# Kernel tuning notes

Measured on AMD Instinct MI355X. Metric: run time of the kernel, lower is better.

## Reference

```python
import jax, jax.numpy as jnp
import numpy as np

D_MODEL = 512
N_HEADS = 8
MAX_CH = 128
LN_EPS = 1e-5


def setup_inputs() -> dict:
    key = jax.random.key(0)
    ks = jax.random.split(key, 8)
    B, T, C, D = 8, 256, 64, D_MODEL
    x = jax.random.normal(ks[0], (B, T, C, D), dtype=jnp.float32)
    # nn.MultiheadAttention params: packed in_proj [3D, D], out_proj [D, D]
    in_proj_w = jax.random.normal(ks[1], (3 * D, D), dtype=jnp.float32) * 0.02
    in_proj_b = jnp.zeros((3 * D,), dtype=jnp.float32)
    out_proj_w = jax.random.normal(ks[2], (D, D), dtype=jnp.float32) * 0.02
    out_proj_b = jnp.zeros((D,), dtype=jnp.float32)
    ln_g = jnp.ones((D,), dtype=jnp.float32)
    ln_b = jnp.zeros((D,), dtype=jnp.float32)
    rel_pos_bias = jax.random.normal(ks[3], (N_HEADS, MAX_CH, MAX_CH), dtype=jnp.float32) * 0.02
    return {"x": x, "in_proj_w": in_proj_w, "in_proj_b": in_proj_b,
            "out_proj_w": out_proj_w, "out_proj_b": out_proj_b,
            "ln_g": ln_g, "ln_b": ln_b, "rel_pos_bias": rel_pos_bias}


def _layernorm(x, g, b):
    mu = jnp.mean(x, axis=-1, keepdims=True)
    var = jnp.var(x, axis=-1, keepdims=True)
    return (x - mu) * jax.lax.rsqrt(var + LN_EPS) * g + b


def reference(x, in_proj_w, in_proj_b, out_proj_w, out_proj_b, ln_g, ln_b, rel_pos_bias):
    B, T, C, D = x.shape
    H = N_HEADS
    hd = D // H
    N = B * T
    xf = x.reshape(N, C, D)
    # 2D additive attn_mask: mean over heads of rel-pos bias, broadcast over heads/batch
    bias = jnp.mean(rel_pos_bias[:, :C, :C], axis=0)  # [C, C]
    qkv = xf @ in_proj_w.T + in_proj_b  # [N, C, 3D]
    q, k, v = jnp.split(qkv, 3, axis=-1)
    q = q.reshape(N, C, H, hd)
    k = k.reshape(N, C, H, hd)
    v = v.reshape(N, C, H, hd)
    scores = jnp.einsum('nqhd,nkhd->nhqk', q, k) / jnp.sqrt(jnp.float32(hd))
    scores = scores + bias[None, None, :, :]
    attn = jax.nn.softmax(scores, axis=-1)
    ctx = jnp.einsum('nhqk,nkhd->nqhd', attn, v).reshape(N, C, D)
    attn_out = ctx @ out_proj_w.T + out_proj_b
    out = _layernorm(xf + attn_out, ln_g, ln_b)
    return out.reshape(B, T, C, D)
```

## Files before the change

kernel.cpp:

```cpp
#include <hip/hip_runtime.h>
#include <stdint.h>
#include <stddef.h>


typedef __attribute__((ext_vector_type(8))) short short8;
typedef __attribute__((ext_vector_type(4))) float f32x4;

typedef __attribute__((address_space(3))) unsigned int as3_u32;
typedef __attribute__((address_space(1))) unsigned int as1_u32;

#define VMCNT8 asm volatile("s_waitcnt vmcnt(8)" ::: "memory")
#define VMCNT5 asm volatile("s_waitcnt vmcnt(5)" ::: "memory")
#define VMCNT4 asm volatile("s_waitcnt vmcnt(4)" ::: "memory")
#define VMCNT0 asm volatile("s_waitcnt vmcnt(0)" ::: "memory")
#define LGKM0  asm volatile("s_waitcnt lgkmcnt(0)" ::: "memory")
#define BARR() __builtin_amdgcn_s_barrier()
#define PRIO1  __builtin_amdgcn_s_setprio(1)
#define PRIO0  __builtin_amdgcn_s_setprio(0)

__device__ __forceinline__ unsigned short f2bf(float f) {
  unsigned u = __builtin_bit_cast(unsigned, f);
  u = (u + 0x7FFFu + ((u >> 16) & 1u)) >> 16;
  return (unsigned short)u;
}

__device__ __forceinline__ f32x4 mfma16(short8 a, short8 b, f32x4 c) {
  return __builtin_amdgcn_mfma_f32_16x16x32_bf16(a, b, c, 0, 0, 0);
}

__device__ __forceinline__ short8 rd8s(const char* buf, int row, int unit) {
  return *(const short8*)(buf + row * 128 + ((unit ^ (row & 7)) * 16));
}
__device__ __forceinline__ void wr2s(char* buf, int row, int col, unsigned short v) {
  int slot = (col >> 3) ^ (row & 7);
  *(unsigned short*)(buf + row * 128 + slot * 16 + (col & 7) * 2) = v;
}
__device__ __forceinline__ void wr8s(char* buf, int row, int col, uint2 v) {
  int slot = (col >> 3) ^ (row & 7);
  *(uint2*)(buf + row * 128 + slot * 16 + (col & 7) * 2) = v;
}

__device__ __forceinline__ void stage16k(char* ldsbase, const char* gsrc, int w, int lane) {
#pragma unroll
  for (int j = 0; j < 4; ++j) {
    int off = j * 4096 + w * 1024;
    __builtin_amdgcn_global_load_lds((const as1_u32*)(gsrc + off + lane * 16),
                                     (as3_u32*)(ldsbase + off), 16, 0, 0);
  }
}

__global__ void prep_kernel(const float* __restrict__ wqkv_f,
                            const float* __restrict__ wo_f,
                            const float* __restrict__ rel,
                            unsigned short* __restrict__ wt,
                            float* __restrict__ bias2d) {
  int b = blockIdx.x, tid = threadIdx.x;
  if (b < 128) {
    unsigned short* dst = wt + (size_t)b * 8192;
#pragma unroll
    for (int t = 0; t < 4; ++t) {
      int u = t * 256 + tid;
      int row = u >> 4, us = u & 15;
      int kg = (us & 8) | ((us ^ row) & 7);
      const float* src;
      if (b < 96) {
        int h = b / 12, i = b % 12;
        int rg = i >> 2, kc = i & 3;
        src = wqkv_f + (size_t)(rg * 512 + h * 64 + row) * 512 + kc * 128 + kg * 8;
      } else {
        int cw = b - 96;
        int kc = cw >> 3, ng = cw & 7;
        src = wo_f + (size_t)(ng * 64 + row) * 512 + kc * 128 + kg * 8;
      }
      float4 a = *(const float4*)src;
      float4 c = *(const float4*)(src + 4);
      unsigned p0 = (unsigned)f2bf(a.x) | ((unsigned)f2bf(a.y) << 16);
      unsigned p1 = (unsigned)f2bf(a.z) | ((unsigned)f2bf(a.w) << 16);
      unsigned p2 = (unsigned)f2bf(c.x) | ((unsigned)f2bf(c.y) << 16);
      unsigned p3 = (unsigned)f2bf(c.z) | ((unsigned)f2bf(c.w) << 16);
      *(uint4*)(dst + u * 8) = make_uint4(p0, p1, p2, p3);
    }
  } else {
    int idx = (b - 128) * 256 + tid;
    int m = idx >> 6, nn = idx & 63;
    float s = 0.f;
#pragma unroll
    for (int hh = 0; hh < 8; ++hh) s += rel[hh * 16384 + m * 128 + nn];
    bias2d[idx] = s * 0.125f;
  }
}

__global__ __launch_bounds__(256)
__attribute__((amdgpu_waves_per_eu(2, 2))) void attn_qkv(
    const float* __restrict__ x,
    const char* __restrict__ wq,
    const float* __restrict__ bqkv,
    const float* __restrict__ bias2d,
    char* __restrict__ ctxg) {
  extern __shared__ __attribute__((aligned(16))) char smem[];
  char* WS = smem;
  char* B0 = smem + 49152;
  char* B1 = smem + 57344;
  char* B2 = smem + 65536;
  float* BQ = (float*)(smem + 73728);

  const int n = blockIdx.x;
  const int tid = threadIdx.x;
  const int w = tid >> 6, lane = tid & 63;
  const int l15 = lane & 15, g = lane >> 4;
  const int wm = w >> 1, wn = w & 1;
  const int mrow = w * 16 + g * 4;
  const int wrow = w * 16 + l15;

#pragma unroll
  for (int i = 0; i < 6; ++i) BQ[i * 256 + tid] = bqkv[i * 256 + tid];

  short8 xf[32];
#pragma unroll
  for (int mt = 0; mt < 2; ++mt) {
    const float* xr = x + ((size_t)n * 64 + wm * 32 + mt * 16 + l15) * 512;
#pragma unroll
    for (int kk = 0; kk < 16; ++kk) {
      float4 a = *(const float4*)(xr + kk * 32 + g * 8);
      float4 c = *(const float4*)(xr + kk * 32 + g * 8 + 4);
      short8 s;
      s[0] = (short)f2bf(a.x); s[1] = (short)f2bf(a.y);
      s[2] = (short)f2bf(a.z); s[3] = (short)f2bf(a.w);
      s[4] = (short)f2bf(c.x); s[5] = (short)f2bf(c.y);
      s[6] = (short)f2bf(c.z); s[7] = (short)f2bf(c.w);
      xf[mt * 16 + kk] = s;
    }
  }
  float b2d[16];
#pragma unroll
  for (int nt = 0; nt < 4; ++nt)
#pragma unroll
    for (int r = 0; r < 4; ++r)
      b2d[nt * 4 + r] = bias2d[(mrow + r) * 64 + nt * 16 + l15];

  LGKM0; BARR();

  stage16k(WS, wq, w, lane);
  stage16k(WS + 16384, wq + 16384, w, lane);

  int b = 0, cur = 0;
  for (int h = 0; h < 8; ++h) {
    float bq2[2], bk2[2], bv2[2];
#pragma unroll
    for (int nt = 0; nt < 2; ++nt) {
      int col = h * 64 + wn * 32 + nt * 16 + l15;
      bq2[nt] = BQ[col];
      bk2[nt] = BQ[512 + col];
      bv2[nt] = BQ[1024 + col];
    }
#pragma unroll
    for (int rg = 0; rg < 3; ++rg) {
      f32x4 acc[2][2] = {};
#pragma unroll
      for (int c = 0; c < 4; ++c) {
        int tgt = cur + 2; if (tgt >= 3) tgt -= 3;
        if (b + 2 < 96) {
          stage16k(WS + tgt * 16384, wq + (size_t)(b + 2) * 16384, w, lane);
          VMCNT8;
        } else if (b + 1 < 96) { VMCNT4; } else { VMCNT0; }
        BARR();
        const char* ws = WS + cur * 16384;
        PRIO1;
#pragma unroll
        for (int ks = 0; ks < 4; ++ks) {
#pragma unroll
          for (int nt = 0; nt < 2; ++nt) {
            int row = wn * 32 + nt * 16 + l15;
            int kg = ks * 4 + g;
            int us = (kg & 8) | ((kg ^ row) & 7);
            short8 bfr = *(const short8*)(ws + row * 256 + us * 16);
            acc[0][nt] = mfma16(xf[c * 4 + ks], bfr, acc[0][nt]);
            acc[1][nt] = mfma16(xf[16 + c * 4 + ks], bfr, acc[1][nt]);
          }
        }
        PRIO0;
        BARR();
        ++b; ++cur; if (cur >= 3) cur -= 3;
      }
      if (rg == 0) {
#pragma unroll
        for (int mt = 0; mt < 2; ++mt)
#pragma unroll
          for (int nt = 0; nt < 2; ++nt)
#pragma unroll
            for (int r = 0; r < 4; ++r)
              wr2s(B0, wm * 32 + mt * 16 + g * 4 + r, wn * 32 + nt * 16 + l15,
                   f2bf(acc[mt][nt][r] + bq2[nt]));
      } else if (rg == 1) {
#pragma unroll
        for (int mt = 0; mt < 2; ++mt)
#pragma unroll
          for (int nt = 0; nt < 2; ++nt)
#pragma unroll
            for (int r = 0; r < 4; ++r)
              wr2s(B1, wm * 32 + mt * 16 + g * 4 + r, wn * 32 + nt * 16 + l15,
                   f2bf(acc[mt][nt][r] + bk2[nt]));
      } else {
#pragma unroll
        for (int mt = 0; mt < 2; ++mt)
#pragma unroll
          for (int nt = 0; nt < 2; ++nt) {
            unsigned short p0 = f2bf(acc[mt][nt][0] + bv2[nt]);
            unsigned short p1 = f2bf(acc[mt][nt][1] + bv2[nt]);
            unsigned short p2 = f2bf(acc[mt][nt][2] + bv2[nt]);
            unsigned short p3 = f2bf(acc[mt][nt][3] + bv2[nt]);
            unsigned lo = (unsigned)p0 | ((unsigned)p1 << 16);
            unsigned hi = (unsigned)p2 | ((unsigned)p3 << 16);
            wr8s(B2, wn * 32 + nt * 16 + l15, wm * 32 + mt * 16 + g * 4,
                 make_uint2(lo, hi));
          }
      }
    }
    LGKM0; BARR();

    {
      f32x4 sc[4] = {};
      short8 aq0 = rd8s(B0, wrow, g);
      short8 aq1 = rd8s(B0, wrow, 4 + g);
#pragma unroll
      for (int nt = 0; nt < 4; ++nt)
        sc[nt] = mfma16(aq0, rd8s(B1, nt * 16 + l15, g), sc[nt]);
#pragma unroll
      for (int nt = 0; nt < 4; ++nt)
        sc[nt] = mfma16(aq1, rd8s(B1, nt * 16 + l15, 4 + g), sc[nt]);
      float mx[4] = {-1e30f, -1e30f, -1e30f, -1e30f};
#pragma unroll
      for (int nt = 0; nt < 4; ++nt)
#pragma unroll
        for (int r = 0; r < 4; ++r) {
          float v = sc[nt][r] * 0.125f + b2d[nt * 4 + r];
          sc[nt][r] = v;
          mx[r] = fmaxf(mx[r], v);
        }
#pragma unroll
      for (int mk = 1; mk < 16; mk <<= 1)
#pragma unroll
        for (int r = 0; r < 4; ++r) mx[r] = fmaxf(mx[r], __shfl_xor(mx[r], mk));
      float sm[4] = {0.f, 0.f, 0.f, 0.f};
#pragma unroll
      for (int nt = 0; nt < 4; ++nt)
#pragma unroll
        for (int r = 0; r < 4; ++r) {
          float e = __expf(sc[nt][r] - mx[r]);
          sc[nt][r] = e;
          sm[r] += e;
        }
#pragma unroll
      for (int mk = 1; mk < 16; mk <<= 1)
#pragma unroll
        for (int r = 0; r < 4; ++r) sm[r] += __shfl_xor(sm[r], mk);
      float inv[4];
#pragma unroll
      for (int r = 0; r < 4; ++r) inv[r] = 1.0f / sm[r];
#pragma unroll
      for (int nt = 0; nt < 4; ++nt)
#pragma unroll
        for (int r = 0; r < 4; ++r)
          wr2s(B0, mrow + r, nt * 16 + l15, f2bf(sc[nt][r] * inv[r]));
    }

    f32x4 cv[4] = {};
    {
      short8 ap0 = rd8s(B0, wrow, g);
      short8 ap1 = rd8s(B0, wrow, 4 + g);
#pragma unroll
      for (int nt = 0; nt < 4; ++nt)
        cv[nt] = mfma16(ap0, rd8s(B2, nt * 16 + l15, g), cv[nt]);
#pragma unroll
      for (int nt = 0; nt < 4; ++nt)
        cv[nt] = mfma16(ap1, rd8s(B2, nt * 16 + l15, 4 + g), cv[nt]);
    }
    BARR();
#pragma unroll
    for (int nt = 0; nt < 4; ++nt)
#pragma unroll
      for (int r = 0; r < 4; ++r)
        wr2s(B1, mrow + r, nt * 16 + l15, f2bf(cv[nt][r]));
    LGKM0; BARR();

    {
      char* cdst = ctxg + (size_t)n * 131072 + h * 8192;
#pragma unroll
      for (int it = 0; it < 2; ++it) {
        int flat = it * 256 + tid;
        int row = flat >> 3, s = flat & 7;
        uint4 v = *(const uint4*)(B1 + row * 128 + s * 16);
        *(uint4*)(cdst + row * 128 + s * 16) = v;
      }
    }
  }
}

__global__ __launch_bounds__(256)
__attribute__((amdgpu_waves_per_eu(2, 2))) void oproj_ln(
    const char* __restrict__ ctxg,
    const char* __restrict__ wo,
    const float* __restrict__ bo,
    const float* __restrict__ x,
    const float* __restrict__ lng,
    const float* __restrict__ lnb,
    float* __restrict__ out) {
  __shared__ __attribute__((aligned(16))) char smem[65536];
  char* WB = smem;
  char* CB = smem + 32768;
  float* EP  = (float*)smem;
  float* SM1 = (float*)(smem + 32768);
  float* SM2 = (float*)(smem + 33408);

  const int n = blockIdx.x;
  const int tid = threadIdx.x;
  const int w = tid >> 6, lane = tid & 63;
  const int l15 = lane & 15, g = lane >> 4;
  const int um = w >> 1, un = w & 1;

  const char* cbase = ctxg + (size_t)n * 131072;

  stage16k(CB, cbase, w, lane);
  stage16k(WB, wo, w, lane);

  f32x4 acc[8][2][2] = {};

  for (int kc = 0; kc < 4; ++kc) {
    short8 actx[2][4];
#pragma unroll
    for (int ng = 0; ng < 8; ++ng) {
      int b = kc * 8 + ng;
      if (b < 31)
        stage16k(WB + (((b + 1) & 1) << 14), wo + (size_t)(b + 1) * 16384, w, lane);
      if ((ng & 1) == 0 && kc < 3) {
        int p = ng >> 1;
        int off = p * 4096 + w * 1024;
        __builtin_amdgcn_global_load_lds(
            (const as1_u32*)(cbase + (kc + 1) * 16384 + off + lane * 16),
            (as3_u32*)(CB + (((kc + 1) & 1) << 14) + off), 16, 0, 0);
      }
      if (b < 31) { VMCNT5; } else { VMCNT0; }
      BARR();
      const char* cb = CB + ((kc & 1) << 14);
      if (ng == 0) {
#pragma unroll
        for (int mt = 0; mt < 2; ++mt)
#pragma unroll
          for (int ks = 0; ks < 4; ++ks) {
            int row = um * 32 + mt * 16 + l15;
            int u = ks * 4 + g;
            actx[mt][ks] = *(const short8*)(cb + (u >> 3) * 8192 + row * 128 +
                                            (((u & 7) ^ (row & 7)) * 16));
          }
      }
      const char* ws = WB + ((b & 1) << 14);
      PRIO1;
#pragma unroll
      for (int ks = 0; ks < 4; ++ks) {
#pragma unroll
        for (int nt = 0; nt < 2; ++nt) {
          int row = un * 32 + nt * 16 + l15;
          int kg = ks * 4 + g;
          int us = (kg & 8) | ((kg ^ row) & 7);
          short8 bfr = *(const short8*)(ws + row * 256 + us * 16);
          acc[ng][0][nt] = mfma16(actx[0][ks], bfr, acc[ng][0][nt]);
          acc[ng][1][nt] = mfma16(actx[1][ks], bfr, acc[ng][1][nt]);
        }
      }
      PRIO0;
      BARR();
    }
  }

  VMCNT0;
  const float* xblk = x + (size_t)n * 32768;
  float* oblk = out + (size_t)n * 32768;
  float s1[2][4] = {}, s2[2][4] = {};

#pragma unroll
  for (int ng = 0; ng < 8; ++ng) {
#pragma unroll
    for (int t = 0; t < 4; ++t) {
      int flat = t * 256 + tid;
      int row = flat >> 4, f4 = flat & 15;
      float4 v = *(const float4*)(xblk + row * 512 + ng * 64 + f4 * 4);
      *(float4*)(EP + row * 68 + f4 * 4) = v;
    }
    LGKM0; BARR();
    float boA[2];
#pragma unroll
    for (int nt = 0; nt < 2; ++nt) boA[nt] = bo[ng * 64 + un * 32 + nt * 16 + l15];
#pragma unroll
    for (int mt = 0; mt < 2; ++mt)
#pragma unroll
      for (int nt = 0; nt < 2; ++nt)
#pragma unroll
        for (int r = 0; r < 4; ++r) {
          int row = um * 32 + mt * 16 + g * 4 + r;
          float xv = EP[row * 68 + un * 32 + nt * 16 + l15];
          float v = acc[ng][mt][nt][r] + boA[nt] + xv;
          acc[ng][mt][nt][r] = v;
          s1[mt][r] += v;
          s2[mt][r] += v * v;
        }
    LGKM0; BARR();
  }
#pragma unroll
  for (int mk = 1; mk < 16; mk <<= 1)
#pragma unroll
    for (int mt = 0; mt < 2; ++mt)
#pragma unroll
      for (int r = 0; r < 4; ++r) {
        s1[mt][r] += __shfl_xor(s1[mt][r], mk);
        s2[mt][r] += __shfl_xor(s2[mt][r], mk);
      }
  if (l15 == 0) {
#pragma unroll
    for (int mt = 0; mt < 2; ++mt)
#pragma unroll
      for (int r = 0; r < 4; ++r) {
        int row = um * 32 + mt * 16 + g * 4 + r;
        SM1[row * 2 + un] = s1[mt][r];
        SM2[row * 2 + un] = s2[mt][r];
      }
  }
  LGKM0; BARR();
  float mu[2][4], rs[2][4];
#pragma unroll
  for (int mt = 0; mt < 2; ++mt)
#pragma unroll
    for (int r = 0; r < 4; ++r) {
      int row = um * 32 + mt * 16 + g * 4 + r;
      float a1 = SM1[row * 2] + SM1[row * 2 + 1];
      float a2 = SM2[row * 2] + SM2[row * 2 + 1];
      float m = a1 * (1.0f / 512.0f);
      float var = a2 * (1.0f / 512.0f) - m * m;
      mu[mt][r] = m;
      rs[mt][r] = rsqrtf(var + 1e-5f);
    }
  BARR();
#pragma unroll
  for (int ng = 0; ng < 8; ++ng) {
    float lgA[2], lbA[2];
#pragma unroll
    for (int nt = 0; nt < 2; ++nt) {
      int col = ng * 64 + un * 32 + nt * 16 + l15;
      lgA[nt] = lng[col];
      lbA[nt] = lnb[col];
    }
#pragma unroll
    for (int mt = 0; mt < 2; ++mt)
#pragma unroll
      for (int nt = 0; nt < 2; ++nt)
#pragma unroll
        for (int r = 0; r < 4; ++r) {
          int row = um * 32 + mt * 16 + g * 4 + r;
          EP[row * 68 + un * 32 + nt * 16 + l15] =
              (acc[ng][mt][nt][r] - mu[mt][r]) * rs[mt][r] * lgA[nt] + lbA[nt];
        }
    LGKM0; BARR();
#pragma unroll
    for (int t = 0; t < 4; ++t) {
      int flat = t * 256 + tid;
      int row = flat >> 4, f4 = flat & 15;
      *(float4*)(oblk + row * 512 + ng * 64 + f4 * 4) =
          *(const float4*)(EP + row * 68 + f4 * 4);
    }
    BARR();
  }
}

extern "C" void kernel_launch(void* const* d_in, const int* in_sizes, int n_in,
                              void* d_out, int out_size, void* d_ws, size_t ws_size,
                              hipStream_t stream) {
  const float* x    = (const float*)d_in[0];
  const float* wqkv = (const float*)d_in[1];
  const float* bqkv = (const float*)d_in[2];
  const float* wo   = (const float*)d_in[3];
  const float* bo   = (const float*)d_in[4];
  const float* lng  = (const float*)d_in[5];
  const float* lnb  = (const float*)d_in[6];
  const float* rel  = (const float*)d_in[7];

  unsigned short* wt = (unsigned short*)d_ws;
  float* bias2d = (float*)((char*)d_ws + 128 * 16384);
  const char* wqc = (const char*)d_ws;
  const char* woc = (const char*)d_ws + 96 * 16384;

  hipFuncSetAttribute(reinterpret_cast<const void*>(attn_qkv),
                      hipFuncAttributeMaxDynamicSharedMemorySize, 79872);

  prep_kernel<<<144, 256, 0, stream>>>(wqkv, wo, rel, wt, bias2d);
  attn_qkv<<<2048, 256, 79872, stream>>>(x, wqc, bqkv, bias2d, (char*)d_out);
  oproj_ln<<<2048, 256, 0, stream>>>((const char*)d_out, woc, bo, x, lng, lnb,
                                     (float*)d_out);
}
```

Baseline: 559.4 us.

## Pre-convert x to bf16 in prep kernel and stream it through LDS

Moves the fp32-to-bf16 conversion of x into the prep kernel, which writes a swizzled bf16 copy into the scratch half of the output buffer. The attention kernel then streams x k-chunks through LDS instead of holding 32 short8 x fragments in registers. It reorders the QKV GEMM so q, k and v accumulate together per k-chunk with double-buffered weight staging. This frees registers and drops the per-block conversion, at the cost of an extra global write and read of x in bf16, more barriers and full vmcnt(0) waits that weaken the prefetch overlap.

```diff
diff --git a/kernel.cpp b/kernel.cpp
--- a/kernel.cpp
+++ b/kernel.cpp
@@ -9,9 +9,7 @@
 typedef __attribute__((address_space(3))) unsigned int as3_u32;
 typedef __attribute__((address_space(1))) unsigned int as1_u32;
 
-#define VMCNT8 asm volatile("s_waitcnt vmcnt(8)" ::: "memory")
 #define VMCNT5 asm volatile("s_waitcnt vmcnt(5)" ::: "memory")
-#define VMCNT4 asm volatile("s_waitcnt vmcnt(4)" ::: "memory")
 #define VMCNT0 asm volatile("s_waitcnt vmcnt(0)" ::: "memory")
 #define LGKM0  asm volatile("s_waitcnt lgkmcnt(0)" ::: "memory")
 #define BARR() __builtin_amdgcn_s_barrier()
@@ -49,29 +47,25 @@
   }
 }
 
-__global__ void prep_kernel(const float* __restrict__ wqkv_f,
+__global__ void prep_kernel(const float* __restrict__ x,
+                            const float* __restrict__ wqkv_f,
                             const float* __restrict__ wo_f,
                             const float* __restrict__ rel,
                             unsigned short* __restrict__ wt,
-                            float* __restrict__ bias2d) {
+                            float* __restrict__ bias2d,
+                            char* __restrict__ dout) {
   int b = blockIdx.x, tid = threadIdx.x;
-  if (b < 128) {
-    unsigned short* dst = wt + (size_t)b * 8192;
+  if (b < 8192) {
+    int n = b >> 2, kc = b & 3;
+    unsigned short* dst =
+        (unsigned short*)(dout + (size_t)n * 131072 + 65536 + kc * 16384);
+    const float* src0 = x + (size_t)n * 32768 + kc * 128;
 #pragma unroll
     for (int t = 0; t < 4; ++t) {
       int u = t * 256 + tid;
       int row = u >> 4, us = u & 15;
       int kg = (us & 8) | ((us ^ row) & 7);
-      const float* src;
-      if (b < 96) {
-        int h = b / 12, i = b % 12;
-        int rg = i >> 2, kc = i & 3;
-        src = wqkv_f + (size_t)(rg * 512 + h * 64 + row) * 512 + kc * 128 + kg * 8;
-      } else {
-        int cw = b - 96;
-        int kc = cw >> 3, ng = cw & 7;
-        src = wo_f + (size_t)(ng * 64 + row) * 512 + kc * 128 + kg * 8;
-      }
+      const float* src = src0 + row * 512 + kg * 8;
       float4 a = *(const float4*)src;
       float4 c = *(const float4*)(src + 4);
       unsigned p0 = (unsigned)f2bf(a.x) | ((unsigned)f2bf(a.y) << 16);
@@ -80,8 +74,34 @@
       unsigned p3 = (unsigned)f2bf(c.z) | ((unsigned)f2bf(c.w) << 16);
       *(uint4*)(dst + u * 8) = make_uint4(p0, p1, p2, p3);
     }
+  } else if (b < 8320) {
+    int cb = b - 8192;
+    unsigned short* dst = wt + (size_t)cb * 8192;
+#pragma unroll
+    for (int t = 0; t < 4; ++t) {
+      int u = t * 256 + tid;
+      int row = u >> 4, us = u & 15;
+      int kg = (us & 8) | ((us ^ row) & 7);
+      const float* src;
+      if (cb < 96) {
+        int h = cb / 12, j = cb % 12;
+        int kc = j / 3, rg = j % 3;
+        src = wqkv_f + (size_t)(rg * 512 + h * 64 + row) * 512 + kc * 128 + kg * 8;
+      } else {
+        int cw = cb - 96;
+        int kc = cw >> 3, ng = cw & 7;
+        src = wo_f + (size_t)(ng * 64 + row) * 512 + kc * 128 + kg * 8;
+      }
+      float4 a = *(const float4*)src;
+      float4 c = *(const float4*)(src + 4);
+      unsigned p0 = (unsigned)f2bf(a.x) | ((unsigned)f2bf(a.y) << 16);
+      unsigned p1 = (unsigned)f2bf(a.z) | ((unsigned)f2bf(a.w) << 16);
+      unsigned p2 = (unsigned)f2bf(c.x) | ((unsigned)f2bf(c.y) << 16);
+      unsigned p3 = (unsigned)f2bf(c.z) | ((unsigned)f2bf(c.w) << 16);
+      *(uint4*)(dst + u * 8) = make_uint4(p0, p1, p2, p3);
+    }
   } else {
-    int idx = (b - 128) * 256 + tid;
+    int idx = (b - 8320) * 256 + tid;
     int m = idx >> 6, nn = idx & 63;
     float s = 0.f;
 #pragma unroll
@@ -90,15 +110,14 @@
   }
 }
 
-__global__ __launch_bounds__(256)
-__attribute__((amdgpu_waves_per_eu(2, 2))) void attn_qkv(
-    const float* __restrict__ x,
+__global__ __launch_bounds__(256, 2) void attn_qkv(
     const char* __restrict__ wq,
     const float* __restrict__ bqkv,
     const float* __restrict__ bias2d,
     char* __restrict__ ctxg) {
   extern __shared__ __attribute__((aligned(16))) char smem[];
-  char* WS = smem;
+  char* WSw = smem;
+  char* WSx = smem + 32768;
   char* B0 = smem + 49152;
   char* B1 = smem + 57344;
   char* B2 = smem + 65536;
@@ -112,25 +131,11 @@
   const int mrow = w * 16 + g * 4;
   const int wrow = w * 16 + l15;
 
+  const char* xsrc = ctxg + (size_t)n * 131072 + 65536;
+
 #pragma unroll
   for (int i = 0; i < 6; ++i) BQ[i * 256 + tid] = bqkv[i * 256 + tid];
 
-  short8 xf[32];
-#pragma unroll
-  for (int mt = 0; mt < 2; ++mt) {
-    const float* xr = x + ((size_t)n * 64 + wm * 32 + mt * 16 + l15) * 512;
-#pragma unroll
-    for (int kk = 0; kk < 16; ++kk) {
-      float4 a = *(const float4*)(xr + kk * 32 + g * 8);
-      float4 c = *(const float4*)(xr + kk * 32 + g * 8 + 4);
-      short8 s;
-      s[0] = (short)f2bf(a.x); s[1] = (short)f2bf(a.y);
-      s[2] = (short)f2bf(a.z); s[3] = (short)f2bf(a.w);
-      s[4] = (short)f2bf(c.x); s[5] = (short)f2bf(c.y);
-      s[6] = (short)f2bf(c.z); s[7] = (short)f2bf(c.w);
-      xf[mt * 16 + kk] = s;
-    }
-  }
   float b2d[16];
 #pragma unroll
   for (int nt = 0; nt < 4; ++nt)
@@ -140,81 +145,116 @@
 
   LGKM0; BARR();
 
-  stage16k(WS, wq, w, lane);
-  stage16k(WS + 16384, wq + 16384, w, lane);
-
-  int b = 0, cur = 0;
+  stage16k(WSw, wq, w, lane);
+  stage16k(WSx, xsrc, w, lane);
+
   for (int h = 0; h < 8; ++h) {
-    float bq2[2], bk2[2], bv2[2];
-#pragma unroll
-    for (int nt = 0; nt < 2; ++nt) {
-      int col = h * 64 + wn * 32 + nt * 16 + l15;
-      bq2[nt] = BQ[col];
-      bk2[nt] = BQ[512 + col];
-      bv2[nt] = BQ[1024 + col];
-    }
-#pragma unroll
-    for (int rg = 0; rg < 3; ++rg) {
-      f32x4 acc[2][2] = {};
-#pragma unroll
-      for (int c = 0; c < 4; ++c) {
-        int tgt = cur + 2; if (tgt >= 3) tgt -= 3;
-        if (b + 2 < 96) {
-          stage16k(WS + tgt * 16384, wq + (size_t)(b + 2) * 16384, w, lane);
-          VMCNT8;
-        } else if (b + 1 < 96) { VMCNT4; } else { VMCNT0; }
-        BARR();
-        const char* ws = WS + cur * 16384;
+    f32x4 aq[2][2] = {}, ak[2][2] = {}, av[2][2] = {};
+#pragma unroll
+    for (int kc = 0; kc < 4; ++kc) {
+      const int b0 = h * 12 + kc * 3;
+      VMCNT0; BARR();
+      short8 xq[8];
+#pragma unroll
+      for (int mt = 0; mt < 2; ++mt)
+#pragma unroll
+        for (int ks = 0; ks < 4; ++ks) {
+          int row = wm * 32 + mt * 16 + l15;
+          int u = ks * 4 + g;
+          int us = (u & 8) | ((u ^ row) & 7);
+          xq[mt * 4 + ks] = *(const short8*)(WSx + row * 256 + us * 16);
+        }
+      if (b0 + 1 < 96) stage16k(WSw + ((b0 + 1) & 1) * 16384,
+                                wq + (size_t)(b0 + 1) * 16384, w, lane);
+      {
+        const char* ws = WSw + (b0 & 1) * 16384;
         PRIO1;
 #pragma unroll
-        for (int ks = 0; ks < 4; ++ks) {
+        for (int ks = 0; ks < 4; ++ks)
 #pragma unroll
           for (int nt = 0; nt < 2; ++nt) {
             int row = wn * 32 + nt * 16 + l15;
             int kg = ks * 4 + g;
             int us = (kg & 8) | ((kg ^ row) & 7);
             short8 bfr = *(const short8*)(ws + row * 256 + us * 16);
-            acc[0][nt] = mfma16(xf[c * 4 + ks], bfr, acc[0][nt]);
-            acc[1][nt] = mfma16(xf[16 + c * 4 + ks], bfr, acc[1][nt]);
+            aq[0][nt] = mfma16(xq[ks], bfr, aq[0][nt]);
+            aq[1][nt] = mfma16(xq[4 + ks], bfr, aq[1][nt]);
           }
-        }
         PRIO0;
-        BARR();
-        ++b; ++cur; if (cur >= 3) cur -= 3;
-      }
-      if (rg == 0) {
-#pragma unroll
-        for (int mt = 0; mt < 2; ++mt)
-#pragma unroll
-          for (int nt = 0; nt < 2; ++nt)
-#pragma unroll
-            for (int r = 0; r < 4; ++r)
-              wr2s(B0, wm * 32 + mt * 16 + g * 4 + r, wn * 32 + nt * 16 + l15,
-                   f2bf(acc[mt][nt][r] + bq2[nt]));
-      } else if (rg == 1) {
-#pragma unroll
-        for (int mt = 0; mt < 2; ++mt)
-#pragma unroll
-          for (int nt = 0; nt < 2; ++nt)
-#pragma unroll
-            for (int r = 0; r < 4; ++r)
-              wr2s(B1, wm * 32 + mt * 16 + g * 4 + r, wn * 32 + nt * 16 + l15,
-                   f2bf(acc[mt][nt][r] + bk2[nt]));
-      } else {
-#pragma unroll
-        for (int mt = 0; mt < 2; ++mt)
+      }
+      BARR();
+      VMCNT0; BARR();
+      if (b0 + 2 < 96) stage16k(WSw + ((b0 + 2) & 1) * 16384,
+                                wq + (size_t)(b0 + 2) * 16384, w, lane);
+      if (!(h == 7 && kc == 3))
+        stage16k(WSx, xsrc + (size_t)((kc + 1) & 3) * 16384, w, lane);
+      {
+        const char* ws = WSw + ((b0 + 1) & 1) * 16384;
+        PRIO1;
+#pragma unroll
+        for (int ks = 0; ks < 4; ++ks)
 #pragma unroll
           for (int nt = 0; nt < 2; ++nt) {
-            unsigned short p0 = f2bf(acc[mt][nt][0] + bv2[nt]);
-            unsigned short p1 = f2bf(acc[mt][nt][1] + bv2[nt]);
-            unsigned short p2 = f2bf(acc[mt][nt][2] + bv2[nt]);
-            unsigned short p3 = f2bf(acc[mt][nt][3] + bv2[nt]);
-            unsigned lo = (unsigned)p0 | ((unsigned)p1 << 16);
-            unsigned hi = (unsigned)p2 | ((unsigned)p3 << 16);
-            wr8s(B2, wn * 32 + nt * 16 + l15, wm * 32 + mt * 16 + g * 4,
-                 make_uint2(lo, hi));
+            int row = wn * 32 + nt * 16 + l15;
+            int kg = ks * 4 + g;
+            int us = (kg & 8) | ((kg ^ row) & 7);
+            short8 bfr = *(const short8*)(ws + row * 256 + us * 16);
+            ak[0][nt] = mfma16(xq[ks], bfr, ak[0][nt]);
+            ak[1][nt] = mfma16(xq[4 + ks], bfr, ak[1][nt]);
           }
-      }
+        PRIO0;
+      }
+      BARR();
+      VMCNT0; BARR();
+      if (b0 + 3 < 96) stage16k(WSw + ((b0 + 3) & 1) * 16384,
+                                wq + (size_t)(b0 + 3) * 16384, w, lane);
+      {
+        const char* ws = WSw + ((b0 + 2) & 1) * 16384;
+        PRIO1;
+#pragma unroll
+        for (int ks = 0; ks < 4; ++ks)
+#pragma unroll
+          for (int nt = 0; nt < 2; ++nt) {
+            int row = wn * 32 + nt * 16 + l15;
+            int kg = ks * 4 + g;
+            int us = (kg & 8) | ((kg ^ row) & 7);
+            short8 bfr = *(const short8*)(ws + row * 256 + us * 16);
+            av[0][nt] = mfma16(xq[ks], bfr, av[0][nt]);
+            av[1][nt] = mfma16(xq[4 + ks], bfr, av[1][nt]);
+          }
+        PRIO0;
+      }
+      BARR();
+    }
+
+    {
+      float bq2[2], bk2[2], bv2[2];
+#pragma unroll
+      for (int nt = 0; nt < 2; ++nt) {
+        int col = h * 64 + wn * 32 + nt * 16 + l15;
+        bq2[nt] = BQ[col];
+        bk2[nt] = BQ[512 + col];
+        bv2[nt] = BQ[1024 + col];
+      }
+#pragma unroll
+      for (int mt = 0; mt < 2; ++mt)
+#pragma unroll
+        for (int nt = 0; nt < 2; ++nt) {
+          int rowb = wm * 32 + mt * 16 + g * 4;
+          int col = wn * 32 + nt * 16 + l15;
+#pragma unroll
+          for (int r = 0; r < 4; ++r) {
+            wr2s(B0, rowb + r, col, f2bf(aq[mt][nt][r] + bq2[nt]));
+            wr2s(B1, rowb + r, col, f2bf(ak[mt][nt][r] + bk2[nt]));
+          }
+          unsigned short p0 = f2bf(av[mt][nt][0] + bv2[nt]);
+          unsigned short p1 = f2bf(av[mt][nt][1] + bv2[nt]);
+          unsigned short p2 = f2bf(av[mt][nt][2] + bv2[nt]);
+          unsigned short p3 = f2bf(av[mt][nt][3] + bv2[nt]);
+          unsigned lo = (unsigned)p0 | ((unsigned)p1 << 16);
+          unsigned hi = (unsigned)p2 | ((unsigned)p3 << 16);
+          wr8s(B2, col, rowb, make_uint2(lo, hi));
+        }
     }
     LGKM0; BARR();
 
@@ -296,8 +336,7 @@
   }
 }
 
-__global__ __launch_bounds__(256)
-__attribute__((amdgpu_waves_per_eu(2, 2))) void oproj_ln(
+__global__ __launch_bounds__(256, 2) void oproj_ln(
     const char* __restrict__ ctxg,
     const char* __restrict__ wo,
     const float* __restrict__ bo,
@@ -490,8 +529,9 @@
   hipFuncSetAttribute(reinterpret_cast<const void*>(attn_qkv),
                       hipFuncAttributeMaxDynamicSharedMemorySize, 79872);
 
-  prep_kernel<<<144, 256, 0, stream>>>(wqkv, wo, rel, wt, bias2d);
-  attn_qkv<<<2048, 256, 79872, stream>>>(x, wqc, bqkv, bias2d, (char*)d_out);
+  prep_kernel<<<8336, 256, 0, stream>>>(x, wqkv, wo, rel, wt, bias2d,
+                                        (char*)d_out);
+  attn_qkv<<<2048, 256, 79872, stream>>>(wqc, bqkv, bias2d, (char*)d_out);
   oproj_ln<<<2048, 256, 0, stream>>>((const char*)d_out, woc, bo, x, lng, lnb,
                                      (float*)d_out);
 }
```

New measurement: 574.8 us. 1.03x slower.
